# Kernel optimization log

Hardware: AMD Instinct MI355X
Metric: run time of the kernel (lower is better)

The kernel has to match this reference:

```python
import jax, jax.numpy as jnp
import numpy as np

VOC_SIZE = 50000
WORD_DIM = 64
CPR_DIM = 64
NUM_RELS = 7
BATCH = 1024
N_LEAVES = 64  # complete binary tree, depth 6
BOUND = 0.05


def setup_inputs() -> dict:
    key = jax.random.key(0)
    ks = jax.random.split(key, 16)
    u = lambda k, shape: jax.random.uniform(k, shape, jnp.float32, -BOUND, BOUND)
    return {
        "left_leaves": jax.random.randint(ks[0], (BATCH, N_LEAVES), 0, VOC_SIZE),
        "right_leaves": jax.random.randint(ks[1], (BATCH, N_LEAVES), 0, VOC_SIZE),
        "voc_w": u(ks[2], (WORD_DIM, VOC_SIZE)),
        "voc_b": u(ks[3], (WORD_DIM,)),
        "cps_w": u(ks[4], (WORD_DIM, 2 * WORD_DIM)),
        "cps_b": u(ks[5], (WORD_DIM,)),
        "cpst_w": u(ks[6], (WORD_DIM, WORD_DIM * WORD_DIM)),
        "cpst_b": u(ks[7], (WORD_DIM,)),
        "cpr_w": u(ks[8], (CPR_DIM, 2 * WORD_DIM)),
        "cpr_b": u(ks[9], (CPR_DIM,)),
        "cprt_w": u(ks[10], (CPR_DIM, WORD_DIM * WORD_DIM)),
        "cprt_b": u(ks[11], (CPR_DIM,)),
        "sm_w": u(ks[12], (NUM_RELS, CPR_DIM)),
        "sm_b": u(ks[13], (NUM_RELS,)),
    }


def _compose(x, cps_w, cps_b, cpst_w, cpst_b):
    # x: [B, N, d] leaf embeddings of a complete binary tree; reduce level by level.
    B, N, d = x.shape
    while N > 1:
        L = x[:, 0::2, :]  # [B, N/2, d]
        R = x[:, 1::2, :]
        cps = jnp.einsum("bnf,ef->bne", jnp.concatenate([L, R], axis=-1), cps_w) + cps_b
        # NOTE: source computes ger(left, left) for interior nodes (left with itself)
        kron = (L[:, :, :, None] * L[:, :, None, :]).reshape(B, N // 2, d * d)
        cps_t = jnp.einsum("bnk,ek->bne", kron, cpst_w) + cpst_b
        x = jnp.tanh(cps + cps_t)
        N //= 2
    return x[:, 0, :]  # [B, d]


def reference(left_leaves, right_leaves, voc_w, voc_b, cps_w, cps_b, cpst_w, cpst_b,
              cpr_w, cpr_b, cprt_w, cprt_b, sm_w, sm_b):
    # onehot @ Linear == embedding gather of columns of voc_w, plus bias
    left_emb = voc_w.T[left_leaves] + voc_b    # [B, N, d]
    right_emb = voc_w.T[right_leaves] + voc_b
    l = _compose(left_emb, cps_w, cps_b, cpst_w, cpst_b)   # [B, d]
    r = _compose(right_emb, cps_w, cps_b, cpst_w, cpst_b)  # [B, d]
    cpr = jnp.concatenate([l, r], axis=-1) @ cpr_w.T + cpr_b
    kron = (l[:, :, None] * r[:, None, :]).reshape(l.shape[0], -1)  # [B, d*d]
    cpr_t = kron @ cprt_w.T + cprt_b
    act = jax.nn.leaky_relu(cpr + cpr_t, negative_slope=0.01)
    logits = act @ sm_w.T + sm_b
    return jax.nn.softmax(logits, axis=-1)  # [B, num_rels]
```

## Files before the change

kernel.cpp:

```cpp
#include <hip/hip_runtime.h>
#include <hip/hip_bf16.h>
#include <cstdint>
#include <cstddef>

typedef _Float16 f16x8 __attribute__((ext_vector_type(8)));
typedef float    f32x4 __attribute__((ext_vector_type(4)));

#define VOC    50000
#define W2T    2432
#define NSTG_T 19
#define W2F    4224
#define NSTG_F 33
#define STG    8192
#define XSTR   72
#define TPW    8
#define IPW    16

__device__ __attribute__((aligned(256))) unsigned short g_vocT[(size_t)VOC * 64];
__device__ __attribute__((aligned(256))) unsigned short g_roots[2048 * 64];
__device__ __attribute__((aligned(256))) unsigned short g_cpstU[(size_t)NSTG_T * STG];
__device__ __attribute__((aligned(256))) unsigned short g_cprtU[(size_t)NSTG_F * STG];
__device__ float g_smw[7 * 64];
__device__ float g_smb[7];
__device__ float g_biasC[64];
__device__ float g_biasF[64];

#define KE(BI0,BJ0,R0,BI1,BJ1,R1) \
    ((BI0) | ((BJ0) << 3) | ((R0) << 6) | ((BI1) << 7) | ((BJ1) << 10) | ((R1) << 13))
__device__ __constant__ int g_ktab[18] = {
    KE(0,0,1, 0,1,1), KE(0,2,0, 0,3,0), KE(0,4,0, 0,5,0), KE(0,6,0, 0,7,0),
    KE(1,1,1, 1,2,1), KE(1,3,0, 1,4,0), KE(1,5,0, 1,6,0), KE(1,7,0, 2,2,1),
    KE(2,3,1, 2,4,0), KE(2,5,0, 2,6,0), KE(2,7,0, 3,3,1), KE(3,4,1, 3,5,0),
    KE(3,6,0, 3,7,0), KE(4,4,1, 4,5,1), KE(4,6,0, 4,7,0), KE(5,5,1, 5,6,1),
    KE(5,7,0, 6,6,1), KE(6,7,1, 7,7,1)
};

__device__ __forceinline__ float b2f(unsigned short u) {
    unsigned int x = ((unsigned int)u) << 16;
    return __builtin_bit_cast(float, x);
}
__device__ __forceinline__ unsigned short f2b(float f) {
    return __builtin_bit_cast(unsigned short, (__bf16)f);
}
__device__ __forceinline__ unsigned short f2h(float f) {
    return __builtin_bit_cast(unsigned short, (_Float16)f);
}
__device__ __forceinline__ float scrub(float v) {
    return fminf(fmaxf(v, -64.f), 64.f);
}
__device__ __forceinline__ float ldf(const void* p, size_t i, int isb) {
    return isb ? b2f(((const unsigned short*)p)[i]) : ((const float*)p)[i];
}
__device__ __forceinline__ int detect_isb(const void* voc_b) {
    const unsigned int* p = (const unsigned int*)voc_b;
    int ok = 1;
    for (int k = 0; k < 32; k++) {
        float v = b2f((unsigned short)(p[k] & 0xFFFFu));
        if (!(fabsf(v) <= 0.0502f)) ok = 0;
    }
    return ok;
}
__device__ __forceinline__ void gload16(const unsigned short* g, unsigned short* l) {
    __builtin_amdgcn_global_load_lds(
        (const __attribute__((address_space(1))) void*)g,
        (__attribute__((address_space(3))) void*)l, 16, 0, 0);
}

__global__ __launch_bounds__(256) void k_prep(
    const void* voc_w, const void* voc_b,
    const void* cps_w, const void* cps_b, const void* cpst_w, const void* cpst_b,
    const void* cpr_w, const void* cpr_b, const void* cprt_w, const void* cprt_b,
    const void* sm_w, const void* sm_b)
{
    __shared__ float tile[64][65];
    __shared__ float vb[64];
    const int isb = detect_isb(voc_b);
    if (blockIdx.x < 512) {
        int gid = blockIdx.x * 256 + threadIdx.x;
        int stride = 512 * 256;
        for (int d = gid; d < 64 * W2T; d += stride) {
            int s    = d / STG;
            int rem  = d - s * STG;
            int kbl  = rem >> 11;
            int rem2 = rem & 2047;
            int nt   = rem2 >> 9;
            int rem3 = rem2 & 511;
            int q    = rem3 >> 7;
            int rem4 = rem3 & 127;
            int sub  = rem4 >> 3;
            int z    = rem4 & 7;
            int n    = nt * 16 + sub;
            int k    = s * 128 + kbl * 32 + q * 8 + z;
            float w;
            if (k < 2304) {
                int b   = k >> 6;
                int p2l = (k >> 5) & 1;
                int bi = 0, remb = b;
                while (remb >= 8 - bi) { remb -= 8 - bi; bi++; }
                int bj = bi + remb;
                int i = bi * 8 + z;
                int j = bj * 8 + 2 * q + p2l;
                w = ldf(cpst_w, (size_t)n * 4096 + i * 64 + j, isb);
                if (bi != bj)
                    w += ldf(cpst_w, (size_t)n * 4096 + j * 64 + i, isb);
            } else {
                w = ldf(cps_w, (size_t)n * 128 + (k - 2304), isb);
            }
            g_cpstU[d] = f2h(w);
        }
        for (int d = gid; d < 64 * W2F; d += stride) {
            int s    = d / STG;
            int rem  = d - s * STG;
            int kbl  = rem >> 11;
            int rem2 = rem & 2047;
            int nt   = rem2 >> 9;
            int rem3 = rem2 & 511;
            int q    = rem3 >> 7;
            int rem4 = rem3 & 127;
            int sub  = rem4 >> 3;
            int z    = rem4 & 7;
            int n    = nt * 16 + sub;
            int k    = s * 128 + kbl * 32 + q * 8 + z;
            float v2 = (k < 4096) ? ldf(cprt_w, (size_t)n * 4096 + k, isb)
                                  : ldf(cpr_w,  (size_t)n * 128 + (k - 4096), isb);
            g_cprtU[d] = f2h(v2);
        }
        for (int i = gid; i < 448; i += stride) g_smw[i] = ldf(sm_w, i, isb);
        if (gid < 64) {
            g_biasC[gid] = ldf(cps_b, gid, isb) + ldf(cpst_b, gid, isb);
            g_biasF[gid] = ldf(cpr_b, gid, isb) + ldf(cprt_b, gid, isb);
        }
        if (gid < 7) g_smb[gid] = ldf(sm_b, gid, isb);
    } else {
        int t = threadIdx.x;
        if (t < 64) vb[t] = ldf(voc_b, t, isb);
        int v0 = (blockIdx.x - 512) * 64;
        int vl = t & 63, dr = t >> 6;
        #pragma unroll
        for (int i = 0; i < 16; i++) {
            int d = dr * 16 + i;
            int v = v0 + vl;
            tile[vl][d] = (v < VOC) ? ldf(voc_w, (size_t)d * VOC + v, isb) : 0.f;
        }
        __syncthreads();
        int dl = t & 63, vr0 = t >> 6;
        #pragma unroll
        for (int i = 0; i < 16; i++) {
            int vr = vr0 * 16 + i;
            int v = v0 + vr;
            if (v < VOC) g_vocT[(size_t)v * 64 + dl] = f2h(tile[vr][dl] + vb[dl]);
        }
    }
}

#define EPILOGUE(CO)                                                          \
    if (lv < 5) {                                                             \
        _Pragma("unroll")                                                     \
        for (int nt = 0; nt < 4; nt++) {                                      \
            int e = nt * 16 + sub;                                            \
            _Pragma("unroll")                                                 \
            for (int rr = 0; rr < 4; rr++) {                                  \
                int m = chv[CO] * 16 + q * 4 + rr;                            \
                if (m < nodes) {                                              \
                    int t2 = m >> lg, n2 = m & (cnew - 1);                    \
                    Xs[(t2 * 64 + n2) * XSTR + e] =                           \
                        f2h(tanhf(scrub(acc[CO][nt][rr] + biasC[e])));        \
                }                                                             \
            }                                                                 \
        }                                                                     \
    } else {                                                                  \
        _Pragma("unroll")                                                     \
        for (int nt = 0; nt < 4; nt++) {                                      \
            int e = nt * 16 + sub;                                            \
            _Pragma("unroll")                                                 \
            for (int rr = 0; rr < 4; rr++) {                                  \
                int m = q * 4 + rr;                                           \
                if (m < TPW)                                                  \
                    g_roots[((size_t)wg * TPW + m) * 64 + e] =                \
                        f2h(tanhf(scrub(acc[CO][nt][rr] + biasC[e])));        \
            }                                                                 \
        }                                                                     \
    }

#define EXSEND(CS)                                                            \
    { _Pragma("unroll")                                                       \
      for (int nt = 0; nt < 4; nt++)                                          \
          *(f32x4*)(exchS + p * 1024 + nt * 256 + lane * 4) = acc[CS][nt]; }

#define EXRECV(CO)                                                            \
    { _Pragma("unroll")                                                       \
      for (int nt = 0; nt < 4; nt++) {                                        \
          f32x4 v_ = *(const f32x4*)(exchS + p * 1024 + nt * 256 + lane * 4); \
          _Pragma("unroll")                                                   \
          for (int z = 0; z < 4; z++) acc[CO][nt][z] += v_[z];                \
      } }

#define KMM(CI, AV, B0, B1, B2, B3)                                           \
    { f16x8 a_ = (AV);                                                        \
      acc[CI][0] = __builtin_amdgcn_mfma_f32_16x16x32_f16(a_, B0, acc[CI][0], 0, 0, 0); \
      acc[CI][1] = __builtin_amdgcn_mfma_f32_16x16x32_f16(a_, B1, acc[CI][1], 0, 0, 0); \
      acc[CI][2] = __builtin_amdgcn_mfma_f32_16x16x32_f16(a_, B2, acc[CI][2], 0, 0, 0); \
      acc[CI][3] = __builtin_amdgcn_mfma_f32_16x16x32_f16(a_, B3, acc[CI][3], 0, 0, 0); }

#define KBLOCK(BP, BI, BJ, RLD)                                               \
    if (act[0]) {                                                             \
        if (RLD) {                                                            \
            lA0 = *(const f16x8*)(Xs + slotL[0] + (BI) * 8);                  \
            if (act[1]) lA1 = *(const f16x8*)(Xs + slotL[1] + (BI) * 8);      \
            if (act[2]) lA2 = *(const f16x8*)(Xs + slotL[2] + (BI) * 8);      \
            if (act[3]) lA3 = *(const f16x8*)(Xs + slotL[3] + (BI) * 8);      \
        }                                                                     \
        _Float16 sc0[4], sc1[4];                                              \
        _Pragma("unroll")                                                     \
        for (int c = 0; c < 4; c++)                                           \
            if (act[c]) {                                                     \
                unsigned pr_ = *(const unsigned*)(Xs + slotL[c] + (BJ) * 8 + 2 * q); \
                sc0[c] = __builtin_bit_cast(_Float16, (unsigned short)(pr_ & 0xFFFFu)); \
                sc1[c] = __builtin_bit_cast(_Float16, (unsigned short)(pr_ >> 16));     \
            }                                                                 \
        _Pragma("unroll")                                                     \
        for (int p2 = 0; p2 < 2; p2++) {                                      \
            const unsigned short* bb = (BP) + p2 * 2048 + lane * 8;           \
            f16x8 b0 = *(const f16x8*)(bb);                                   \
            f16x8 b1 = *(const f16x8*)(bb + 512);                             \
            f16x8 b2 = *(const f16x8*)(bb + 1024);                            \
            f16x8 b3 = *(const f16x8*)(bb + 1536);                            \
            KMM(0, lA0 * (p2 ? sc1[0] : sc0[0]), b0, b1, b2, b3)              \
            if (act[1]) KMM(1, lA1 * (p2 ? sc1[1] : sc0[1]), b0, b1, b2, b3)  \
            if (act[2]) KMM(2, lA2 * (p2 ? sc1[2] : sc0[2]), b0, b1, b2, b3)  \
            if (act[3]) KMM(3, lA3 * (p2 ? sc1[3] : sc0[3]), b0, b1, b2, b3)  \
        }                                                                     \
    }

#define KRUN(S, BPTR)                                                         \
    {                                                                         \
        int e_   = g_ktab[S];                                                 \
        int ent_ = half ? (e_ >> 7) : e_;                                     \
        int bi_  = ent_ & 7;                                                  \
        int bj_  = (ent_ >> 3) & 7;                                           \
        int rld_ = (ent_ >> 6) & 1;                                           \
        KBLOCK((BPTR), bi_, bj_, rld_)                                        \
    }

__global__ __launch_bounds__(512, 2)
void k_tree(const int* __restrict__ lleaf, const int* __restrict__ rleaf)
{
    __shared__ __attribute__((aligned(16))) unsigned short Xs[512 * XSTR];
    __shared__ __attribute__((aligned(16))) unsigned short Bsup[2][2 * STG];
    __shared__ __attribute__((aligned(16))) float exchS[4096];
    __shared__ float biasC[64];
    const int tid = threadIdx.x;
    const int wg  = blockIdx.x;

    #pragma unroll
    for (int j = 0; j < 4; j++)
        gload16(g_cpstU + j * 4096 + (size_t)tid * 8, Bsup[0] + j * 4096 + tid * 8);

    if (tid < 64) biasC[tid] = g_biasC[tid];

    {
        int t = tid >> 6, i = tid & 63;
        int gidx = wg * TPW + t;
        int b = (gidx < 1024) ? gidx : gidx - 1024;
        const int* lv2 = (gidx < 1024) ? lleaf : rleaf;
        int idx = lv2[b * 64 + i];
        idx = (idx < 0) ? 0 : ((idx >= VOC) ? VOC - 1 : idx);
        const uint4* src = (const uint4*)(g_vocT + (size_t)idx * 64);
        uint4* dst = (uint4*)(Xs + tid * XSTR);
        #pragma unroll
        for (int z = 0; z < 8; z++) dst[z] = src[z];
    }

    __syncthreads();

    const int lane = tid & 63, wave = tid >> 6;
    const int q = lane >> 4, sub = lane & 15;
    const int p = wave >> 1, half = wave & 1;

    #pragma unroll 1
    for (int lv = 0; lv < 6; lv++) {
        const int lg = 5 - lv;
        const int cnew = 1 << lg;
        const int nodes = TPW << lg;
        const int nchunks = (nodes + 15) >> 4;

        int act[4], chv[4], slotL[4];
        #pragma unroll
        for (int c = 0; c < 4; c++) {
            int ch = p + 4 * c;
            act[c] = (ch < nchunks);
            chv[c] = ch;
            int m = ch * 16 + sub;
            if (!act[c] || m >= nodes) m = 0;
            int t = m >> lg, n = m & (cnew - 1);
            slotL[c] = (t * 64 + 2 * n) * XSTR;
        }

        f16x8 lA0 = {}, lA1 = {}, lA2 = {}, lA3 = {};
        f32x4 acc[4][4];
        #pragma unroll
        for (int c = 0; c < 4; c++)
            #pragma unroll
            for (int nt = 0; nt < 4; nt++)
                #pragma unroll
                for (int z = 0; z < 4; z++) acc[c][nt][z] = 0.f;

        #pragma unroll 1
        for (int t = 0; t < 9; t++) {
            if (t < 8) {
                const unsigned short* ksrc = g_cpstU + (size_t)(2 * t + 2) * STG;
                unsigned short* kdst = Bsup[(t + 1) & 1];
                #pragma unroll
                for (int j = 0; j < 4; j++)
                    gload16(ksrc + j * 4096 + (size_t)tid * 8, kdst + j * 4096 + tid * 8);
            } else {
                const unsigned short* ksrc = g_cpstU + (size_t)18 * STG;
                #pragma unroll
                for (int j = 0; j < 2; j++)
                    gload16(ksrc + j * 4096 + (size_t)tid * 8, Bsup[1] + j * 4096 + tid * 8);
            }
            const unsigned short* Bp = Bsup[t & 1] + (half << 12);
            KRUN(2 * t,     Bp)
            KRUN(2 * t + 1, Bp + STG)
            __syncthreads();
        }

        {
            const unsigned short* Bp = Bsup[1] + (half << 12);
            if (lv < 5) {
                #pragma unroll
                for (int j = 0; j < 4; j++)
                    gload16(g_cpstU + j * 4096 + (size_t)tid * 8, Bsup[0] + j * 4096 + tid * 8);
            }
            if (act[0]) {
                #pragma unroll
                for (int p2 = 0; p2 < 2; p2++) {
                    const unsigned short* bb = Bp + p2 * 2048 + lane * 8;
                    f16x8 b0 = *(const f16x8*)(bb);
                    f16x8 b1 = *(const f16x8*)(bb + 512);
                    f16x8 b2 = *(const f16x8*)(bb + 1024);
                    f16x8 b3 = *(const f16x8*)(bb + 1536);
                    #pragma unroll
                    for (int c = 0; c < 4; c++) {
                        if (!act[c]) continue;
                        f16x8 A = *(const f16x8*)(Xs + slotL[c] + half * XSTR + p2 * 32 + q * 8);
                        acc[c][0] = __builtin_amdgcn_mfma_f32_16x16x32_f16(A, b0, acc[c][0], 0, 0, 0);
                        acc[c][1] = __builtin_amdgcn_mfma_f32_16x16x32_f16(A, b1, acc[c][1], 0, 0, 0);
                        acc[c][2] = __builtin_amdgcn_mfma_f32_16x16x32_f16(A, b2, acc[c][2], 0, 0, 0);
                        acc[c][3] = __builtin_amdgcn_mfma_f32_16x16x32_f16(A, b3, acc[c][3], 0, 0, 0);
                    }
                }
            }
            __syncthreads();
        }

        if (half == 0) { if (act[1]) EXSEND(1) } else { if (act[0]) EXSEND(0) }
        __syncthreads();
        if (half == 0) {
            if (act[0]) { EXRECV(0) EPILOGUE(0) }
        } else {
            if (act[1]) { EXRECV(1) EPILOGUE(1) }
        }
        __syncthreads();
        if (half == 0) { if (act[3]) EXSEND(3) } else { if (act[2]) EXSEND(2) }
        __syncthreads();
        if (half == 0) {
            if (act[2]) { EXRECV(2) EPILOGUE(2) }
        } else {
            if (act[3]) { EXRECV(3) EPILOGUE(3) }
        }
        __syncthreads();
    }
}

#define FKRON(S, BPTR)                                                        \
    { _Pragma("unroll")                                                       \
      for (int ii = 0; ii < 2; ii++) {                                        \
          int i_ = 2 * (S) + ii;                                              \
          _Float16 li_ = __builtin_bit_cast(_Float16, Lv[rowLo + i_]);        \
          _Pragma("unroll")                                                   \
          for (int p2 = 0; p2 < 2; p2++) {                                    \
              f16x8 bfr_ = *(const f16x8*)((BPTR) + (2 * ii + p2) * 2048 + w * 512 + lane * 8); \
              f16x8 afr_ = Ra[p2] * li_;                                      \
              acc = __builtin_amdgcn_mfma_f32_16x16x32_f16(afr_, bfr_, acc, 0, 0, 0); \
          }                                                                   \
      } }

__global__ __launch_bounds__(256, 2) void k_final(const void* __restrict__ voc_b,
                                                  void* __restrict__ out)
{
    __shared__ __attribute__((aligned(16))) unsigned short Lv[IPW * XSTR], Rv[IPW * XSTR];
    __shared__ __attribute__((aligned(16))) unsigned short Bsup[2][2 * STG];
    __shared__ float actS[IPW][65];
    __shared__ float smw[7][64];
    __shared__ float smbS[7];
    __shared__ float biasF[64];
    const int tid = threadIdx.x, wg = blockIdx.x;
    const int isb = detect_isb(voc_b);

    #pragma unroll
    for (int j = 0; j < 8; j++)
        gload16(g_cprtU + j * 2048 + (size_t)tid * 8, Bsup[0] + j * 2048 + tid * 8);

    if (tid < 64) biasF[tid] = g_biasF[tid];
    if (tid < 7)  smbS[tid] = g_smb[tid];
    for (int z = tid; z < 448; z += 256) smw[z >> 6][z & 63] = g_smw[z];

    {
        int side = tid >> 7, idx = tid & 127;
        int item = idx >> 3, piece = idx & 7;
        const uint4* s4 = (const uint4*)(g_roots +
            ((size_t)(side * 1024) + (size_t)wg * IPW + item) * 64 + piece * 8);
        uint4* d4 = (uint4*)((side ? Rv : Lv) + item * XSTR + piece * 8);
        *d4 = *s4;
    }

    __syncthreads();

    const int lane = tid & 63, w = tid >> 6;
    const int q = lane >> 4, sub = lane & 15;
    const int rowLo = sub * XSTR;

    f16x8 Ra[2];
    Ra[0] = *(const f16x8*)(Rv + rowLo + q * 8);
    Ra[1] = *(const f16x8*)(Rv + rowLo + 32 + q * 8);

    f32x4 acc;
    #pragma unroll
    for (int z = 0; z < 4; z++) acc[z] = 0.f;

    #pragma unroll 1
    for (int t = 0; t < 16; t++) {
        if (t < 15) {
            const unsigned short* src = g_cprtU + (size_t)(2 * t + 2) * STG;
            unsigned short* dst = Bsup[(t + 1) & 1];
            #pragma unroll
            for (int j = 0; j < 8; j++)
                gload16(src + j * 2048 + (size_t)tid * 8, dst + j * 2048 + tid * 8);
        } else {
            const unsigned short* src = g_cprtU + (size_t)32 * STG;
            #pragma unroll
            for (int j = 0; j < 4; j++)
                gload16(src + j * 2048 + (size_t)tid * 8, Bsup[0] + j * 2048 + tid * 8);
        }
        const unsigned short* Bp = Bsup[t & 1];
        FKRON(2 * t,     Bp)
        FKRON(2 * t + 1, Bp + STG)
        __syncthreads();
    }

    {
        const unsigned short* Bp = Bsup[0];
        f16x8 A4[4];
        A4[0] = *(const f16x8*)(Lv + rowLo + q * 8);
        A4[1] = *(const f16x8*)(Lv + rowLo + 32 + q * 8);
        A4[2] = *(const f16x8*)(Rv + rowLo + q * 8);
        A4[3] = *(const f16x8*)(Rv + rowLo + 32 + q * 8);
        #pragma unroll
        for (int kbl = 0; kbl < 4; kbl++) {
            f16x8 bfr = *(const f16x8*)(Bp + kbl * 2048 + w * 512 + lane * 8);
            acc = __builtin_amdgcn_mfma_f32_16x16x32_f16(A4[kbl], bfr, acc, 0, 0, 0);
        }
    }

    {
        int e = w * 16 + sub;
        #pragma unroll
        for (int rr = 0; rr < 4; rr++) {
            int item = q * 4 + rr;
            float v = scrub(acc[rr] + biasF[e]);
            v = (v > 0.f) ? v : 0.01f * v;
            actS[item][e] = v;
        }
    }
    __syncthreads();

    if (tid < IPW) {
        float lg[7];
        #pragma unroll
        for (int j = 0; j < 7; j++) lg[j] = smbS[j];
        for (int e = 0; e < 64; e++) {
            float a = actS[tid][e];
            #pragma unroll
            for (int j = 0; j < 7; j++) lg[j] += smw[j][e] * a;
        }
        float mx = lg[0];
        #pragma unroll
        for (int j = 1; j < 7; j++) mx = fmaxf(mx, lg[j]);
        float s = 0.f, pr[7];
        #pragma unroll
        for (int j = 0; j < 7; j++) { pr[j] = expf(lg[j] - mx); s += pr[j]; }
        float inv = 1.f / s;
        size_t b = (size_t)wg * IPW + tid;
        if (isb) {
            unsigned short* o = (unsigned short*)out;
            #pragma unroll
            for (int j = 0; j < 7; j++) o[b * 7 + j] = f2b(pr[j] * inv);
        } else {
            float* o = (float*)out;
            #pragma unroll
            for (int j = 0; j < 7; j++) o[b * 7 + j] = pr[j] * inv;
        }
    }
}

extern "C" void kernel_launch(void* const* d_in, const int* in_sizes, int n_in,
                              void* d_out, int out_size, void* d_ws, size_t ws_size,
                              hipStream_t stream) {
    const int* lleaf = (const int*)d_in[0];
    const int* rleaf = (const int*)d_in[1];
    const void* voc_w  = d_in[2];
    const void* voc_b  = d_in[3];
    const void* cps_w  = d_in[4];
    const void* cps_b  = d_in[5];
    const void* cpst_w = d_in[6];
    const void* cpst_b = d_in[7];
    const void* cpr_w  = d_in[8];
    const void* cpr_b  = d_in[9];
    const void* cprt_w = d_in[10];
    const void* cprt_b = d_in[11];
    const void* sm_w   = d_in[12];
    const void* sm_b   = d_in[13];

    k_prep<<<512 + (VOC + 63) / 64, 256, 0, stream>>>(
        voc_w, voc_b, cps_w, cps_b, cpst_w, cpst_b,
        cpr_w, cpr_b, cprt_w, cprt_b, sm_w, sm_b);
    k_tree<<<2048 / TPW, 512, 0, stream>>>(lleaf, rleaf);
    k_final<<<64, 256, 0, stream>>>(voc_b, (unsigned short*)d_out);
}
```

Before: 199.0 us.

## Load weight fragments directly from global into registers, dropping LDS staging

Both the tree-compose and final kernels stop staging the Kronecker weight matrices through double-buffered LDS with async global-to-LDS loads and per-stage barriers. Each wave instead loads its own B fragments straight from global (L2-resident) memory into registers, ping-ponging between two register sets. The cross-wave exchange buffer is enlarged so each wave writes its own slot and reads its partner's. This removes the barriers and frees LDS, at the cost of more register pressure and global/L2 load latency sitting in the MFMA loop.

```diff
diff --git a/kernel.cpp b/kernel.cpp
--- a/kernel.cpp
+++ b/kernel.cpp
@@ -59,11 +59,6 @@
         if (!(fabsf(v) <= 0.0502f)) ok = 0;
     }
     return ok;
-}
-__device__ __forceinline__ void gload16(const unsigned short* g, unsigned short* l) {
-    __builtin_amdgcn_global_load_lds(
-        (const __attribute__((address_space(1))) void*)g,
-        (__attribute__((address_space(3))) void*)l, 16, 0, 0);
 }
 
 __global__ __launch_bounds__(256) void k_prep(
@@ -185,15 +180,21 @@
 #define EXSEND(CS)                                                            \
     { _Pragma("unroll")                                                       \
       for (int nt = 0; nt < 4; nt++)                                          \
-          *(f32x4*)(exchS + p * 1024 + nt * 256 + lane * 4) = acc[CS][nt]; }
+          *(f32x4*)(exchS + wave * 1024 + nt * 256 + lane * 4) = acc[CS][nt]; }
 
 #define EXRECV(CO)                                                            \
     { _Pragma("unroll")                                                       \
       for (int nt = 0; nt < 4; nt++) {                                        \
-          f32x4 v_ = *(const f32x4*)(exchS + p * 1024 + nt * 256 + lane * 4); \
+          f32x4 v_ = *(const f32x4*)(exchS + (wave ^ 1) * 1024 + nt * 256 + lane * 4); \
           _Pragma("unroll")                                                   \
           for (int z = 0; z < 4; z++) acc[CO][nt][z] += v_[z];                \
       } }
+
+#define BLD8(BF, SBASE)                                                       \
+    { const unsigned short* gs_ = (SBASE) + half * 4096 + lane * 8;           \
+      _Pragma("unroll")                                                       \
+      for (int j = 0; j < 8; j++)                                             \
+          BF[j] = *(const f16x8*)(gs_ + (j >> 2) * 2048 + (j & 3) * 512); }
 
 #define KMM(CI, AV, B0, B1, B2, B3)                                           \
     { f16x8 a_ = (AV);                                                        \
@@ -202,7 +203,7 @@
       acc[CI][2] = __builtin_amdgcn_mfma_f32_16x16x32_f16(a_, B2, acc[CI][2], 0, 0, 0); \
       acc[CI][3] = __builtin_amdgcn_mfma_f32_16x16x32_f16(a_, B3, acc[CI][3], 0, 0, 0); }
 
-#define KBLOCK(BP, BI, BJ, RLD)                                               \
+#define KBLOCKR(BF, BI, BJ, RLD)                                              \
     if (act[0]) {                                                             \
         if (RLD) {                                                            \
             lA0 = *(const f16x8*)(Xs + slotL[0] + (BI) * 8);                  \
@@ -220,41 +221,35 @@
             }                                                                 \
         _Pragma("unroll")                                                     \
         for (int p2 = 0; p2 < 2; p2++) {                                      \
-            const unsigned short* bb = (BP) + p2 * 2048 + lane * 8;           \
-            f16x8 b0 = *(const f16x8*)(bb);                                   \
-            f16x8 b1 = *(const f16x8*)(bb + 512);                             \
-            f16x8 b2 = *(const f16x8*)(bb + 1024);                            \
-            f16x8 b3 = *(const f16x8*)(bb + 1536);                            \
-            KMM(0, lA0 * (p2 ? sc1[0] : sc0[0]), b0, b1, b2, b3)              \
-            if (act[1]) KMM(1, lA1 * (p2 ? sc1[1] : sc0[1]), b0, b1, b2, b3)  \
-            if (act[2]) KMM(2, lA2 * (p2 ? sc1[2] : sc0[2]), b0, b1, b2, b3)  \
-            if (act[3]) KMM(3, lA3 * (p2 ? sc1[3] : sc0[3]), b0, b1, b2, b3)  \
+            KMM(0, lA0 * (p2 ? sc1[0] : sc0[0]),                              \
+                BF[p2 * 4 + 0], BF[p2 * 4 + 1], BF[p2 * 4 + 2], BF[p2 * 4 + 3]) \
+            if (act[1]) KMM(1, lA1 * (p2 ? sc1[1] : sc0[1]),                  \
+                BF[p2 * 4 + 0], BF[p2 * 4 + 1], BF[p2 * 4 + 2], BF[p2 * 4 + 3]) \
+            if (act[2]) KMM(2, lA2 * (p2 ? sc1[2] : sc0[2]),                  \
+                BF[p2 * 4 + 0], BF[p2 * 4 + 1], BF[p2 * 4 + 2], BF[p2 * 4 + 3]) \
+            if (act[3]) KMM(3, lA3 * (p2 ? sc1[3] : sc0[3]),                  \
+                BF[p2 * 4 + 0], BF[p2 * 4 + 1], BF[p2 * 4 + 2], BF[p2 * 4 + 3]) \
         }                                                                     \
     }
 
-#define KRUN(S, BPTR)                                                         \
+#define KRUNR(S, BF)                                                          \
     {                                                                         \
         int e_   = g_ktab[S];                                                 \
         int ent_ = half ? (e_ >> 7) : e_;                                     \
         int bi_  = ent_ & 7;                                                  \
         int bj_  = (ent_ >> 3) & 7;                                           \
         int rld_ = (ent_ >> 6) & 1;                                           \
-        KBLOCK((BPTR), bi_, bj_, rld_)                                        \
+        KBLOCKR((BF), bi_, bj_, rld_)                                         \
     }
 
 __global__ __launch_bounds__(512, 2)
 void k_tree(const int* __restrict__ lleaf, const int* __restrict__ rleaf)
 {
     __shared__ __attribute__((aligned(16))) unsigned short Xs[512 * XSTR];
-    __shared__ __attribute__((aligned(16))) unsigned short Bsup[2][2 * STG];
-    __shared__ __attribute__((aligned(16))) float exchS[4096];
+    __shared__ __attribute__((aligned(16))) float exchS[8192];
     __shared__ float biasC[64];
     const int tid = threadIdx.x;
     const int wg  = blockIdx.x;
-
-    #pragma unroll
-    for (int j = 0; j < 4; j++)
-        gload16(g_cpstU + j * 4096 + (size_t)tid * 8, Bsup[0] + j * 4096 + tid * 8);
 
     if (tid < 64) biasC[tid] = g_biasC[tid];
 
@@ -305,53 +300,29 @@
                 #pragma unroll
                 for (int z = 0; z < 4; z++) acc[c][nt][z] = 0.f;
 
+        f16x8 bfA[8], bfB[8];
+        if (act[0]) BLD8(bfA, g_cpstU)
         #pragma unroll 1
         for (int t = 0; t < 9; t++) {
-            if (t < 8) {
-                const unsigned short* ksrc = g_cpstU + (size_t)(2 * t + 2) * STG;
-                unsigned short* kdst = Bsup[(t + 1) & 1];
+            if (act[0]) BLD8(bfB, g_cpstU + (size_t)(2 * t + 1) * STG)
+            KRUNR(2 * t, bfA)
+            if (act[0]) BLD8(bfA, g_cpstU + (size_t)(2 * t + 2) * STG)
+            KRUNR(2 * t + 1, bfB)
+        }
+
+        if (act[0]) {
+            #pragma unroll
+            for (int p2 = 0; p2 < 2; p2++) {
                 #pragma unroll
-                for (int j = 0; j < 4; j++)
-                    gload16(ksrc + j * 4096 + (size_t)tid * 8, kdst + j * 4096 + tid * 8);
-            } else {
-                const unsigned short* ksrc = g_cpstU + (size_t)18 * STG;
-                #pragma unroll
-                for (int j = 0; j < 2; j++)
-                    gload16(ksrc + j * 4096 + (size_t)tid * 8, Bsup[1] + j * 4096 + tid * 8);
-            }
-            const unsigned short* Bp = Bsup[t & 1] + (half << 12);
-            KRUN(2 * t,     Bp)
-            KRUN(2 * t + 1, Bp + STG)
-            __syncthreads();
-        }
-
-        {
-            const unsigned short* Bp = Bsup[1] + (half << 12);
-            if (lv < 5) {
-                #pragma unroll
-                for (int j = 0; j < 4; j++)
-                    gload16(g_cpstU + j * 4096 + (size_t)tid * 8, Bsup[0] + j * 4096 + tid * 8);
-            }
-            if (act[0]) {
-                #pragma unroll
-                for (int p2 = 0; p2 < 2; p2++) {
-                    const unsigned short* bb = Bp + p2 * 2048 + lane * 8;
-                    f16x8 b0 = *(const f16x8*)(bb);
-                    f16x8 b1 = *(const f16x8*)(bb + 512);
-                    f16x8 b2 = *(const f16x8*)(bb + 1024);
-                    f16x8 b3 = *(const f16x8*)(bb + 1536);
-                    #pragma unroll
-                    for (int c = 0; c < 4; c++) {
-                        if (!act[c]) continue;
-                        f16x8 A = *(const f16x8*)(Xs + slotL[c] + half * XSTR + p2 * 32 + q * 8);
-                        acc[c][0] = __builtin_amdgcn_mfma_f32_16x16x32_f16(A, b0, acc[c][0], 0, 0, 0);
-                        acc[c][1] = __builtin_amdgcn_mfma_f32_16x16x32_f16(A, b1, acc[c][1], 0, 0, 0);
-                        acc[c][2] = __builtin_amdgcn_mfma_f32_16x16x32_f16(A, b2, acc[c][2], 0, 0, 0);
-                        acc[c][3] = __builtin_amdgcn_mfma_f32_16x16x32_f16(A, b3, acc[c][3], 0, 0, 0);
-                    }
+                for (int c = 0; c < 4; c++) {
+                    if (!act[c]) continue;
+                    f16x8 A = *(const f16x8*)(Xs + slotL[c] + half * XSTR + p2 * 32 + q * 8);
+                    acc[c][0] = __builtin_amdgcn_mfma_f32_16x16x32_f16(A, bfA[p2 * 4 + 0], acc[c][0], 0, 0, 0);
+                    acc[c][1] = __builtin_amdgcn_mfma_f32_16x16x32_f16(A, bfA[p2 * 4 + 1], acc[c][1], 0, 0, 0);
+                    acc[c][2] = __builtin_amdgcn_mfma_f32_16x16x32_f16(A, bfA[p2 * 4 + 2], acc[c][2], 0, 0, 0);
+                    acc[c][3] = __builtin_amdgcn_mfma_f32_16x16x32_f16(A, bfA[p2 * 4 + 3], acc[c][3], 0, 0, 0);
                 }
             }
-            __syncthreads();
         }
 
         if (half == 0) { if (act[1]) EXSEND(1) } else { if (act[0]) EXSEND(0) }
@@ -373,16 +344,21 @@
     }
 }
 
-#define FKRON(S, BPTR)                                                        \
+#define BLD4(BF, S)                                                           \
+    { const unsigned short* gs_ = g_cprtU + (size_t)(S) * STG + w * 512 + lane * 8; \
+      _Pragma("unroll")                                                       \
+      for (int j = 0; j < 4; j++)                                             \
+          BF[j] = *(const f16x8*)(gs_ + j * 2048); }
+
+#define FKRONR(S, BF)                                                         \
     { _Pragma("unroll")                                                       \
       for (int ii = 0; ii < 2; ii++) {                                        \
           int i_ = 2 * (S) + ii;                                              \
           _Float16 li_ = __builtin_bit_cast(_Float16, Lv[rowLo + i_]);        \
           _Pragma("unroll")                                                   \
           for (int p2 = 0; p2 < 2; p2++) {                                    \
-              f16x8 bfr_ = *(const f16x8*)((BPTR) + (2 * ii + p2) * 2048 + w * 512 + lane * 8); \
               f16x8 afr_ = Ra[p2] * li_;                                      \
-              acc = __builtin_amdgcn_mfma_f32_16x16x32_f16(afr_, bfr_, acc, 0, 0, 0); \
+              acc = __builtin_amdgcn_mfma_f32_16x16x32_f16(afr_, BF[2 * ii + p2], acc, 0, 0, 0); \
           }                                                                   \
       } }
 
@@ -390,17 +366,12 @@
                                                   void* __restrict__ out)
 {
     __shared__ __attribute__((aligned(16))) unsigned short Lv[IPW * XSTR], Rv[IPW * XSTR];
-    __shared__ __attribute__((aligned(16))) unsigned short Bsup[2][2 * STG];
     __shared__ float actS[IPW][65];
     __shared__ float smw[7][64];
     __shared__ float smbS[7];
     __shared__ float biasF[64];
     const int tid = threadIdx.x, wg = blockIdx.x;
     const int isb = detect_isb(voc_b);
-
-    #pragma unroll
-    for (int j = 0; j < 8; j++)
-        gload16(g_cprtU + j * 2048 + (size_t)tid * 8, Bsup[0] + j * 2048 + tid * 8);
 
     if (tid < 64) biasF[tid] = g_biasF[tid];
     if (tid < 7)  smbS[tid] = g_smb[tid];
@@ -415,12 +386,15 @@
         *d4 = *s4;
     }
 
-    __syncthreads();
-
     const int lane = tid & 63, w = tid >> 6;
     const int q = lane >> 4, sub = lane & 15;
     const int rowLo = sub * XSTR;
 
+    f16x8 bA[4], bB[4];
+    BLD4(bA, 0)
+
+    __syncthreads();
+
     f16x8 Ra[2];
     Ra[0] = *(const f16x8*)(Rv + rowLo + q * 8);
     Ra[1] = *(const f16x8*)(Rv + rowLo + 32 + q * 8);
@@ -431,36 +405,21 @@
 
     #pragma unroll 1
     for (int t = 0; t < 16; t++) {
-        if (t < 15) {
-            const unsigned short* src = g_cprtU + (size_t)(2 * t + 2) * STG;
-            unsigned short* dst = Bsup[(t + 1) & 1];
-            #pragma unroll
-            for (int j = 0; j < 8; j++)
-                gload16(src + j * 2048 + (size_t)tid * 8, dst + j * 2048 + tid * 8);
-        } else {
-            const unsigned short* src = g_cprtU + (size_t)32 * STG;
-            #pragma unroll
-            for (int j = 0; j < 4; j++)
-                gload16(src + j * 2048 + (size_t)tid * 8, Bsup[0] + j * 2048 + tid * 8);
-        }
-        const unsigned short* Bp = Bsup[t & 1];
-        FKRON(2 * t,     Bp)
-        FKRON(2 * t + 1, Bp + STG)
-        __syncthreads();
+        BLD4(bB, 2 * t + 1)
+        FKRONR(2 * t, bA)
+        BLD4(bA, 2 * t + 2)
+        FKRONR(2 * t + 1, bB)
     }
 
     {
-        const unsigned short* Bp = Bsup[0];
         f16x8 A4[4];
         A4[0] = *(const f16x8*)(Lv + rowLo + q * 8);
         A4[1] = *(const f16x8*)(Lv + rowLo + 32 + q * 8);
         A4[2] = *(const f16x8*)(Rv + rowLo + q * 8);
         A4[3] = *(const f16x8*)(Rv + rowLo + 32 + q * 8);
         #pragma unroll
-        for (int kbl = 0; kbl < 4; kbl++) {
-            f16x8 bfr = *(const f16x8*)(Bp + kbl * 2048 + w * 512 + lane * 8);
-            acc = __builtin_amdgcn_mfma_f32_16x16x32_f16(A4[kbl], bfr, acc, 0, 0, 0);
-        }
+        for (int kbl = 0; kbl < 4; kbl++)
+            acc = __builtin_amdgcn_mfma_f32_16x16x32_f16(A4[kbl], bA[kbl], acc, 0, 0, 0);
     }
 
     {
```

Result: faster. 177.3 us (-10.9%).
